# Kernel optimization log

Hardware: AMD Instinct MI355X
Metric: run time of the kernel (lower is better)

Reference implementation:

```python
import jax, jax.numpy as jnp
import numpy as np
from jax import lax

NUM_CLASSES = 80
STRIDES = (8, 16, 32)
CENTER_RADIUS = 2.5
CANDIDATE_K = 10


def setup_inputs() -> dict:
    key = jax.random.key(0)
    ks = jax.random.split(key, 6)
    B, G, NGT = 32, 50, 20
    out0 = jax.random.normal(ks[0], (B, 85, 80, 80), jnp.float32)
    out1 = jax.random.normal(ks[1], (B, 85, 40, 40), jnp.float32)
    out2 = jax.random.normal(ks[2], (B, 85, 20, 20), jnp.float32)
    cls = jax.random.randint(ks[3], (B, G, 1), 0, NUM_CLASSES).astype(jnp.float32)
    cxcy = jax.random.uniform(ks[4], (B, G, 2), minval=32.0, maxval=608.0)
    wh = jax.random.uniform(ks[5], (B, G, 2), minval=16.0, maxval=128.0)
    labels = jnp.concatenate([cls, cxcy, wh], -1)
    valid = (jnp.arange(G) < NGT)[None, :, None]
    labels = labels * valid  # padded rows are all-zero, as the torch code expects
    return {"out0": out0, "out1": out1, "out2": out2, "labels": labels}


def _decode(out, stride):
    # out: [B, 85, H, W] -> [B, H*W, 85] with xy=(pred+grid)*stride, wh=exp(pred)*stride
    B, C, H, W = out.shape
    o = out.transpose(0, 2, 3, 1).reshape(B, H * W, C)
    yv, xv = jnp.meshgrid(jnp.arange(H), jnp.arange(W), indexing="ij")
    grid = jnp.stack([xv, yv], -1).reshape(H * W, 2).astype(out.dtype)
    xy = (o[..., :2] + grid) * stride
    wh = jnp.exp(o[..., 2:4]) * stride
    dec = jnp.concatenate([xy, wh, o[..., 4:]], -1)
    centers = (grid + 0.5) * stride
    strides = jnp.full((H * W,), float(stride), out.dtype)
    return dec, centers, strides


def _pairwise_iou(a, b):
    # a: [G,4] cxcywh, b: [A,4] cxcywh -> [G,A]
    tl = jnp.maximum(a[:, None, :2] - a[:, None, 2:] * 0.5, b[None, :, :2] - b[None, :, 2:] * 0.5)
    br = jnp.minimum(a[:, None, :2] + a[:, None, 2:] * 0.5, b[None, :, :2] + b[None, :, 2:] * 0.5)
    en = jnp.all(tl < br, -1).astype(a.dtype)
    inter = jnp.prod(br - tl, -1) * en
    area_a = a[:, 2] * a[:, 3]
    area_b = b[:, 2] * b[:, 3]
    return inter / (area_a[:, None] + area_b[None, :] - inter + 1e-12)


def _iou_loss(pred, tgt):
    # elementwise IoU loss (YOLOX IOUloss, loss_type='iou'): 1 - iou^2
    tl = jnp.maximum(pred[..., :2] - pred[..., 2:] * 0.5, tgt[..., :2] - tgt[..., 2:] * 0.5)
    br = jnp.minimum(pred[..., :2] + pred[..., 2:] * 0.5, tgt[..., :2] + tgt[..., 2:] * 0.5)
    en = jnp.all(tl < br, -1).astype(pred.dtype)
    inter = jnp.prod(jnp.clip(br - tl, 0.0), -1) * en
    union = pred[..., 2] * pred[..., 3] + tgt[..., 2] * tgt[..., 3] - inter + 1e-16
    iou = inter / union
    return 1.0 - iou * iou


def _bce_logits(x, y):
    return jnp.maximum(x, 0.0) - x * y + jnp.log1p(jnp.exp(-jnp.abs(x)))


def _assign(boxes, cls_logits, obj_logit, labels_b, centers, strides):
    # Per-image SimOTA. boxes [A,4], cls_logits [A,C], obj_logit [A], labels_b [G,5]
    G = labels_b.shape[0]
    gt_valid = labels_b.sum(-1) > 0                       # [G]
    gt_box = labels_b[:, 1:5]                             # [G,4] cxcywh
    gt_cls = labels_b[:, 0].astype(jnp.int32)
    cx, cy = centers[:, 0], centers[:, 1]
    # in-box test (strict, as min(delta)>0 in torch)
    in_box = ((cx[None] > gt_box[:, 0:1] - 0.5 * gt_box[:, 2:3])
              & (cx[None] < gt_box[:, 0:1] + 0.5 * gt_box[:, 2:3])
              & (cy[None] > gt_box[:, 1:2] - 0.5 * gt_box[:, 3:4])
              & (cy[None] < gt_box[:, 1:2] + 0.5 * gt_box[:, 3:4]))  # [G,A]
    rs = CENTER_RADIUS * strides[None]
    in_ctr = ((jnp.abs(cx[None] - gt_box[:, 0:1]) < rs)
              & (jnp.abs(cy[None] - gt_box[:, 1:2]) < rs))           # [G,A]
    fg = jnp.any((in_box | in_ctr) & gt_valid[:, None], axis=0)       # [A]
    geom = in_box & in_ctr                                            # is_in_boxes_and_center
    cand = fg[None, :] & gt_valid[:, None]                            # valid (gt, anchor) pairs

    iou = _pairwise_iou(gt_box, boxes)                                # [G,A]
    iou_m = jnp.where(cand, iou, 0.0)
    iou_cost = -jnp.log(iou + 1e-8)

    # cls cost without materializing [G,A,C]: p = sqrt(sig(cls)*sig(obj));
    # BCE(p, onehot(g)).sum(C) = -log p[g] + log(1-p[g]) - sum_c log(1-p[c])
    p = jnp.sqrt(jax.nn.sigmoid(cls_logits) * jax.nn.sigmoid(obj_logit)[:, None])  # [A,C]
    p = jnp.clip(p, 1e-7, 1.0 - 1e-6)
    logp = jnp.log(p)
    log1mp = jnp.log1p(-p)
    s = log1mp.sum(-1)                                                # [A]
    lp_g = jnp.take(logp, gt_cls, axis=1).T                           # [G,A]
    l1_g = jnp.take(log1mp, gt_cls, axis=1).T                         # [G,A]
    cls_cost = -lp_g + l1_g - s[None, :]

    cost = (cls_cost + 3.0 * iou_cost
            + 100000.0 * (~geom).astype(cost_dtype := boxes.dtype)
            + 1e9 * (~cand).astype(boxes.dtype))

    # dynamic-k: k_g = clamp(int(sum(topk10 ious)), 1)
    topk_ious = lax.top_k(iou_m, CANDIDATE_K)[0]                      # [G,10]
    dyn_k = jnp.clip(topk_ious.sum(-1).astype(jnp.int32), 1, None)    # [G]
    sorted_cost = jnp.sort(cost, axis=1)
    thr = jnp.take_along_axis(sorted_cost, (dyn_k - 1)[:, None], axis=1)
    match = (cost <= thr) & cand                                      # [G,A]

    # resolve anchors matched to multiple gts: keep global argmin-cost gt
    count = match.sum(0)                                              # [A]
    best_gt = jnp.argmin(cost, axis=0)                                # [A]
    keep = jnp.arange(G)[:, None] == best_gt[None, :]
    match = jnp.where(count[None, :] > 1, match & keep, match)

    fg_final = match.any(0)                                           # [A]
    matched_gt = jnp.argmax(match, axis=0)                            # [A]
    pred_iou = (match.astype(iou.dtype) * iou).sum(0)                 # [A]
    return fg_final, matched_gt, pred_iou, gt_valid


def _forward(out0, out1, out2, labels):
    decs, ctrs, strs = [], [], []
    for o, s in zip((out0, out1, out2), STRIDES):
        d, c, st = _decode(o, s)
        decs.append(d); ctrs.append(c); strs.append(st)
    outputs = jnp.concatenate(decs, axis=1)          # [B, A, 85]
    centers = jnp.concatenate(ctrs, axis=0)          # [A, 2]
    strides = jnp.concatenate(strs, axis=0)          # [A]

    bbox = outputs[..., :4]
    obj = outputs[..., 4]
    cls = outputs[..., 5:]

    assign = jax.vmap(_assign, in_axes=(0, 0, 0, 0, None, None))
    fg, mgt, piou, gt_valid = assign(
        lax.stop_gradient(bbox), lax.stop_gradient(cls),
        lax.stop_gradient(obj), lax.stop_gradient(labels), centers, strides)
    piou = lax.stop_gradient(piou)

    gt_box = lax.stop_gradient(labels[:, :, 1:5])
    reg_t = jnp.take_along_axis(gt_box, mgt[..., None], axis=1)       # [B,A,4]
    gt_cls = labels[..., 0].astype(jnp.int32)
    mcls = jnp.take_along_axis(gt_cls, mgt, axis=1)                   # [B,A]
    cls_t = jax.nn.one_hot(mcls, NUM_CLASSES, dtype=outputs.dtype) * piou[..., None]

    fgf = fg.astype(outputs.dtype)
    num_fg = jnp.maximum(fgf.sum(), 1.0)
    loss_iou = (_iou_loss(bbox, reg_t) * fgf).sum() / num_fg
    loss_obj = _bce_logits(obj, fgf).sum() / num_fg
    loss_cls = (_bce_logits(cls, cls_t).sum(-1) * fgf).sum() / num_fg
    return 5.0 * loss_iou + loss_obj + loss_cls


def reference(out0, out1, out2, labels):
    return _forward(out0, out1, out2, labels)
```

## Files before the change

kernel.cpp:

```cpp
#include <hip/hip_runtime.h>
#include <math.h>

#define B_  32
#define A_  8400
#define G_  50
#define NC_ 80
#define PAD 4352
#define CHK_A 33
#define CHK_C 17
#define NBLK_C (8*4*CHK_C)
#define CLIPHI ((float)(1.0 - 1e-6))

#define ACC_NUMFG 0
#define ACC_IOU   32
#define ACC_OBJ0  64
#define ACC_OBJFG 96
#define ACC_CLS   128

struct AInfo { int lvl; int within; int w; int hw; float s; int x; int y; };

__device__ __forceinline__ AInfo anchor_info(int a) {
  AInfo r;
  if (a < 6400)      { r.lvl = 0; r.within = a;        r.w = 80; r.hw = 6400; r.s = 8.0f;  }
  else if (a < 8000) { r.lvl = 1; r.within = a - 6400; r.w = 40; r.hw = 1600; r.s = 16.0f; }
  else               { r.lvl = 2; r.within = a - 8000; r.w = 20; r.hw = 400;  r.s = 32.0f; }
  r.x = r.within % r.w; r.y = r.within / r.w;
  return r;
}

__device__ __forceinline__ const float* lvl_base(const float* o0, const float* o1,
                                                 const float* o2, int lvl) {
  return lvl == 0 ? o0 : (lvl == 1 ? o1 : o2);
}

__device__ __forceinline__ float2 cost_iou(
    float gx, float gy, float gw, float gh,
    float fx, float fy, float st,
    float4 bx, float ssum, float sobj, float clsv)
{
  float cx = (fx + 0.5f) * st;
  float cy = (fy + 0.5f) * st;
  bool in_box = (cx > gx - 0.5f*gw) && (cx < gx + 0.5f*gw) &&
                (cy > gy - 0.5f*gh) && (cy < gy + 0.5f*gh);
  float rs = 2.5f * st;
  bool in_ctr = (fabsf(cx - gx) < rs) && (fabsf(cy - gy) < rs);
  bool geom = in_box && in_ctr;
  float tlx = fmaxf(gx - gw*0.5f, bx.x - bx.z*0.5f);
  float tly = fmaxf(gy - gh*0.5f, bx.y - bx.w*0.5f);
  float brx = fminf(gx + gw*0.5f, bx.x + bx.z*0.5f);
  float bry = fminf(gy + gh*0.5f, bx.y + bx.w*0.5f);
  bool en = (tlx < brx) && (tly < bry);
  float inter = en ? (brx - tlx) * (bry - tly) : 0.0f;
  float iou = inter / (gw*gh + bx.z*bx.w - inter + 1e-12f);
  float iou_cost = -__logf(iou + 1e-8f);
  float sc = 1.0f / (1.0f + __expf(-clsv));
  float p = sqrtf(sc * sobj);
  p = fminf(fmaxf(p, 1e-7f), CLIPHI);
  float cls_cost = -__logf(p) + __logf(1.0f - p) - ssum;
  float cost = cls_cost + 3.0f * iou_cost;
  if (!geom) cost += 100000.0f;
  return make_float2(cost, iou);
}

__global__ __launch_bounds__(256)
void kA(const float* __restrict__ o0, const float* __restrict__ o1,
        const float* __restrict__ o2, const float* __restrict__ labels,
        float4* __restrict__ cBox, float4* __restrict__ cPack,
        int* __restrict__ ncandP, float* __restrict__ accP)
{
  __shared__ float gl[G_], gr[G_], gtt[G_], gbb[G_], gcx[G_], gcy[G_];
  __shared__ int nvgS;
  __shared__ float wsum[4];
  __shared__ int wcnt[4], wbase[4];
  __shared__ int aL[256];
  __shared__ float soL[256], v4L[256];
  int j = blockIdx.x;
  int x8 = j & 7, r = j >> 3;
  int b = x8 + 8*(r & 3);
  int chunk = r >> 2;
  int tid = threadIdx.x;
  if (tid < 64) {
    bool v = false; float l0=0,gx=0,gy=0,gw=0,gh=0;
    if (tid < G_) {
      const float* L = labels + (size_t)b*G_*5 + tid*5;
      l0=L[0]; gx=L[1]; gy=L[2]; gw=L[3]; gh=L[4];
      v = (l0+gx+gy+gw+gh) > 0.0f;
    }
    unsigned long long mm = __ballot(v);
    if (tid == 0) nvgS = __popcll(mm);
    if (v) {
      int pos = __popcll(mm & ((1ull << tid) - 1ull));
      gl[pos]  = gx - 0.5f*gw; gr[pos]  = gx + 0.5f*gw;
      gtt[pos] = gy - 0.5f*gh; gbb[pos] = gy + 0.5f*gh;
      gcx[pos] = gx; gcy[pos] = gy;
    }
  }
  __syncthreads();
  int nvg = nvgS;
  int a = chunk*256 + tid;
  float objbce = 0.0f, v4 = 0.0f, so = 0.0f;
  float4 bx = make_float4(0.f,0.f,0.f,0.f);
  bool anyfg = false;
  if (a < A_) {
    AInfo ai = anchor_info(a);
    const float* base = lvl_base(o0,o1,o2,ai.lvl) + (size_t)b*85*ai.hw + ai.within;
    float v0 = base[0];
    float v1 = base[(size_t)1*ai.hw];
    float v2 = base[(size_t)2*ai.hw];
    float v3 = base[(size_t)3*ai.hw];
    v4 = base[(size_t)4*ai.hw];
    bx.x = (v0 + (float)ai.x) * ai.s;
    bx.y = (v1 + (float)ai.y) * ai.s;
    bx.z = __expf(v2) * ai.s;
    bx.w = __expf(v3) * ai.s;
    objbce = fmaxf(v4, 0.0f) + __logf(1.0f + __expf(-fabsf(v4)));
    float cx = ((float)ai.x + 0.5f) * ai.s;
    float cy = ((float)ai.y + 0.5f) * ai.s;
    float rs = 2.5f * ai.s;
    for (int k = 0; k < nvg; k++) {
      bool in_box = (cx > gl[k]) & (cx < gr[k]) & (cy > gtt[k]) & (cy < gbb[k]);
      bool in_ctr = (fabsf(cx - gcx[k]) < rs) & (fabsf(cy - gcy[k]) < rs);
      anyfg = anyfg | in_box | in_ctr;
    }
    so = 1.0f / (1.0f + __expf(-v4));
  }
  float v = objbce;
  for (int o = 32; o > 0; o >>= 1) v += __shfl_down(v, o, 64);
  int lane = tid & 63, w = tid >> 6;
  if (lane == 0) wsum[w] = v;
  unsigned long long mm = __ballot(anyfg);
  if (lane == 0) wcnt[w] = __popcll(mm);
  __syncthreads();
  if (tid == 0) {
    atomicAdd(&accP[ACC_OBJ0], wsum[0]+wsum[1]+wsum[2]+wsum[3]);
    int t0=wcnt[0], t1=wcnt[1], t2=wcnt[2], t3=wcnt[3];
    int tot = t0+t1+t2+t3;
    int bas = tot ? atomicAdd(&ncandP[b*64], tot) : 0;
    wbase[0]=bas; wbase[1]=bas+t0; wbase[2]=bas+t0+t1; wbase[3]=bas+t0+t1+t2;
  }
  __syncthreads();
  if (anyfg) {
    int pre = __popcll(mm & ((1ull << lane) - 1ull));
    int lpos = (wbase[w] - wbase[0]) + pre;
    aL[lpos] = a; soL[lpos] = so; v4L[lpos] = v4;
    int pos = wbase[w] + pre;
    if (pos < PAD) cBox[b*PAD + pos] = bx;
  }
  __syncthreads();
  int base0 = wbase[0];
  int tot = (wbase[3] + wcnt[3]) - base0;
  for (int t = tid; t < tot; t += 256) {
    if (base0 + t >= PAD) break;
    int a2 = aL[t];
    float so2 = soL[t];
    AInfo ai = anchor_info(a2);
    const float* q = lvl_base(o0,o1,o2,ai.lvl) + (size_t)(b*85 + 5)*ai.hw + ai.within;
    float s0=0,s1=0,s2=0,s3=0,s4=0,s5=0,s6=0,s7=0;
    #pragma unroll
    for (int c = 0; c < NC_; c += 8) {
      float x0 = q[(size_t)(c+0)*ai.hw];
      float x1 = q[(size_t)(c+1)*ai.hw];
      float x2 = q[(size_t)(c+2)*ai.hw];
      float x3 = q[(size_t)(c+3)*ai.hw];
      float x4 = q[(size_t)(c+4)*ai.hw];
      float x5 = q[(size_t)(c+5)*ai.hw];
      float x6 = q[(size_t)(c+6)*ai.hw];
      float x7 = q[(size_t)(c+7)*ai.hw];
      #define TERM(xx, ss_) { \
        float sc = 1.0f/(1.0f+__expf(-(xx))); \
        float p = sqrtf(sc*so2); \
        p = fminf(fmaxf(p,1e-7f), CLIPHI); \
        ss_ += __logf(1.0f - p); }
      TERM(x0,s0) TERM(x1,s1) TERM(x2,s2) TERM(x3,s3)
      TERM(x4,s4) TERM(x5,s5) TERM(x6,s6) TERM(x7,s7)
      #undef TERM
    }
    float ss = ((s0+s1)+(s2+s3)) + ((s4+s5)+(s6+s7));
    cPack[b*PAD + base0 + t] = make_float4(ss, so2, __int_as_float(a2), v4L[t]);
  }
}

__global__ __launch_bounds__(256)
void kB(const float* __restrict__ o0, const float* __restrict__ o1,
        const float* __restrict__ o2, const float* __restrict__ labels,
        const float4* __restrict__ cBox, const float4* __restrict__ cPack,
        const int* __restrict__ ncandP, float* __restrict__ thrw,
        float* __restrict__ costM)
{
  __shared__ float sh[256*10];
  __shared__ int s_dk;
  int j = blockIdx.x;
  int x8 = j & 7, r = j >> 3;
  int b = x8 + 8*(r & 3);
  int g = r >> 2;
  int tid = threadIdx.x;
  const float* L = labels + (size_t)(b*G_ + g)*5;
  float l0=L[0], gx=L[1], gy=L[2], gw=L[3], gh=L[4];
  bool gvalid = (l0+gx+gy+gw+gh) > 0.0f;
  if (!gvalid) { if (tid==0) thrw[b*G_+g] = -3.0e38f; return; }
  int gcls = (int)l0;
  int nc = ncandP[b*64]; if (nc > PAD) nc = PAD;
  float* row = costM + ((size_t)b*G_ + g)*(size_t)PAD;
  float ti[10], tc[10];
  #pragma unroll
  for (int jq=0;jq<10;jq++){ ti[jq]=0.0f; tc[jq]=3e38f; }

  auto body = [&](int i) {
    float4 bx = cBox[b*PAD + i];
    float4 pk = cPack[b*PAD + i];
    int a = __float_as_int(pk.z);
    AInfo ai = anchor_info(a);
    float clsv = lvl_base(o0,o1,o2,ai.lvl)[(size_t)(b*85 + 5 + gcls)*ai.hw + ai.within];
    float2 ci = cost_iou(gx,gy,gw,gh,(float)ai.x,(float)ai.y,ai.s,
                         bx, pk.x, pk.y, clsv);
    row[i] = ci.x;
    float v = ci.y;
    if (v > ti[9]) {
      #pragma unroll
      for (int jq=0;jq<10;jq++){ float o=ti[jq]; bool t=v>o; ti[jq]=t?v:o; v=t?o:v; }
    }
    float c = ci.x;
    if (c < tc[9]) {
      #pragma unroll
      for (int jq=0;jq<10;jq++){ float o=tc[jq]; bool t=c<o; tc[jq]=t?c:o; c=t?o:c; }
    }
  };
  int i = tid;
  for (; i + 256 < nc; i += 512) { body(i); body(i + 256); }
  if (i < nc) body(i);

  #pragma unroll
  for (int jq=0;jq<10;jq++) sh[tid*10+jq] = ti[jq];
  __syncthreads();
  for (int str=128; str>0; str>>=1) {
    if (tid < str) {
      float out[10]; int ii=0, jj=0;
      float* Aa = &sh[tid*10]; float* Bb = &sh[(tid+str)*10];
      #pragma unroll
      for (int k=0;k<10;k++){ float va=Aa[ii], vb=Bb[jj]; bool t=(va>=vb); out[k]=t?va:vb; if(t)ii++; else jj++; }
      #pragma unroll
      for (int k=0;k<10;k++) Aa[k]=out[k];
    }
    __syncthreads();
  }
  if (tid==0) {
    float s10=0.0f;
    #pragma unroll
    for (int jq=0;jq<10;jq++) s10 += sh[jq];
    int dk = (int)s10; if (dk<1) dk=1; if (dk>10) dk=10;
    s_dk = dk;
  }
  __syncthreads();
  #pragma unroll
  for (int jq=0;jq<10;jq++) sh[tid*10+jq] = tc[jq];
  __syncthreads();
  for (int str=128; str>0; str>>=1) {
    if (tid < str) {
      float out[10]; int ii=0, jj=0;
      float* Aa = &sh[tid*10]; float* Bb = &sh[(tid+str)*10];
      #pragma unroll
      for (int k=0;k<10;k++){ float va=Aa[ii], vb=Bb[jj]; bool t=(va<=vb); out[k]=t?va:vb; if(t)ii++; else jj++; }
      #pragma unroll
      for (int k=0;k<10;k++) Aa[k]=out[k];
    }
    __syncthreads();
  }
  if (tid==0) thrw[b*G_+g] = sh[s_dk-1];
}

__global__ __launch_bounds__(256)
void kC(const float* __restrict__ o0, const float* __restrict__ o1,
        const float* __restrict__ o2, const float* __restrict__ labels,
        const float4* __restrict__ cBox, const float4* __restrict__ cPack,
        const int* __restrict__ ncandP, const float* __restrict__ thrw,
        const float* __restrict__ costM, float* __restrict__ accP,
        int* __restrict__ doneP, float* __restrict__ out)
{
  __shared__ float labS[G_*5];
  __shared__ float thrS[G_];
  __shared__ int vgIdx[G_];
  __shared__ int nvgS;
  __shared__ float wpart[4][4];
  __shared__ int aML[256];
  __shared__ float piML[256];
  __shared__ int mclsML[256];
  __shared__ int mcntS;
  int j = blockIdx.x;
  int x8 = j & 7, r = j >> 3;
  int b = x8 + 8*(r & 3);
  int chunk = r >> 2;
  int tid = threadIdx.x;
  int nc = ncandP[b*64]; if (nc > PAD) nc = PAD;
  bool active = (chunk*256 < nc);
  if (active) {
    for (int i = tid; i < G_*5; i += 256) labS[i] = labels[(size_t)b*G_*5 + i];
    if (tid < G_) thrS[tid] = thrw[b*G_ + tid];
    if (tid == 0) mcntS = 0;
    __syncthreads();
    if (tid < 64) {
      bool v = false;
      if (tid < G_) {
        float s5 = labS[tid*5]+labS[tid*5+1]+labS[tid*5+2]+labS[tid*5+3]+labS[tid*5+4];
        v = (s5 > 0.0f);
      }
      unsigned long long mm = __ballot(v);
      if (tid == 0) nvgS = __popcll(mm);
      if (v) vgIdx[__popcll(mm & ((1ull << tid) - 1ull))] = tid;
    }
    __syncthreads();
    int nvg = nvgS;
    int i = chunk*256 + tid;
    float accPf=0.f, accIou=0.f, accObjx=0.f, accCls=0.f;
    bool matched = false; int m_a = 0; float m_pi = 0.0f; int m_cls = 0;
    if (i < nc) {
      const float* cm = costM + (size_t)b*G_*(size_t)PAD + i;
      float minc = 3e38f; int ming = 0;
      int cnt = 0; int firstg = -1;
      #define PROC(kk, cc) { \
        int g = vgIdx[kk]; \
        if ((cc) < minc) { minc = (cc); ming = g; } \
        if ((cc) <= thrS[g]) { cnt++; if (firstg < 0) firstg = g; } }
      int k = 0;
      for (; k + 4 <= nvg; k += 4) {
        float c0 = cm[(size_t)vgIdx[k+0]*PAD];
        float c1 = cm[(size_t)vgIdx[k+1]*PAD];
        float c2 = cm[(size_t)vgIdx[k+2]*PAD];
        float c3 = cm[(size_t)vgIdx[k+3]*PAD];
        PROC(k+0, c0) PROC(k+1, c1) PROC(k+2, c2) PROC(k+3, c3)
      }
      for (; k < nvg; k++) {
        float c0 = cm[(size_t)vgIdx[k]*PAD];
        PROC(k, c0)
      }
      #undef PROC
      int mg = -1;
      if (cnt == 1)     mg = firstg;
      else if (cnt > 1) { if (minc <= thrS[ming]) mg = ming; }
      if (mg >= 0) {
        float4 bx = cBox[b*PAD + i];
        float4 pk = cPack[b*PAD + i];
        accPf = 1.0f;
        accObjx = pk.w;
        float tx=labS[mg*5+1], ty=labS[mg*5+2], tw=labS[mg*5+3], th=labS[mg*5+4];
        float tlx = fmaxf(tx - tw*0.5f, bx.x - bx.z*0.5f);
        float tly = fmaxf(ty - th*0.5f, bx.y - bx.w*0.5f);
        float brx = fminf(tx + tw*0.5f, bx.x + bx.z*0.5f);
        float bry = fminf(ty + th*0.5f, bx.y + bx.w*0.5f);
        bool en = (tlx < brx) && (tly < bry);
        float inter_p = en ? (brx - tlx) * (bry - tly) : 0.0f;
        float pi = inter_p / (tw*th + bx.z*bx.w - inter_p + 1e-12f);
        float iw = fmaxf(brx-tlx, 0.0f), ih = fmaxf(bry-tly, 0.0f);
        float inter = iw*ih * (en ? 1.0f : 0.0f);
        float uni = bx.z*bx.w + tw*th - inter + 1e-16f;
        float iou2 = inter/uni;
        accIou = 1.0f - iou2*iou2;
        matched = true;
        m_a = __float_as_int(pk.z);
        m_pi = pi;
        m_cls = (int)labS[mg*5];
      }
    }
    {
      int lane = tid & 63;
      unsigned long long mm = __ballot(matched);
      int cnt = __popcll(mm);
      int bpos = 0;
      if (lane == 0 && cnt) bpos = atomicAdd(&mcntS, cnt);
      bpos = __shfl(bpos, 0, 64);
      if (matched) {
        int p = bpos + __popcll(mm & ((1ull << lane) - 1ull));
        aML[p] = m_a; piML[p] = m_pi; mclsML[p] = m_cls;
      }
    }
    __syncthreads();
    {
      int lane = tid & 63, w = tid >> 6;
      int mcount = mcntS;
      for (int idx = w; idx < mcount; idx += 4) {
        int a2 = aML[idx]; float pi2 = piML[idx]; int mc = mclsML[idx];
        AInfo ai = anchor_info(a2);
        const float* clsbase = lvl_base(o0,o1,o2,ai.lvl) + (size_t)(b*85 + 5)*ai.hw + ai.within;
        float x1 = clsbase[(size_t)lane * ai.hw];
        accCls += fmaxf(x1,0.0f) - x1*((lane==mc)?pi2:0.0f) + __logf(1.0f + __expf(-fabsf(x1)));
        if (lane < NC_ - 64) {
          int c2 = lane + 64;
          float x2 = clsbase[(size_t)c2 * ai.hw];
          accCls += fmaxf(x2,0.0f) - x2*((c2==mc)?pi2:0.0f) + __logf(1.0f + __expf(-fabsf(x2)));
        }
      }
    }
    for (int o = 32; o > 0; o >>= 1) {
      accPf   += __shfl_down(accPf,   o, 64);
      accIou  += __shfl_down(accIou,  o, 64);
      accObjx += __shfl_down(accObjx, o, 64);
      accCls  += __shfl_down(accCls,  o, 64);
    }
    int lane = tid & 63, w = tid >> 6;
    if (lane == 0) { wpart[w][0]=accPf; wpart[w][1]=accIou; wpart[w][2]=accObjx; wpart[w][3]=accCls; }
    __syncthreads();
    if (tid == 0) {
      float s0=0.f,s1=0.f,s2=0.f,s3=0.f;
      for (int q=0;q<4;q++){ s0+=wpart[q][0]; s1+=wpart[q][1]; s2+=wpart[q][2]; s3+=wpart[q][3]; }
      if (s0!=0.f) atomicAdd(&accP[ACC_NUMFG], s0);
      if (s1!=0.f) atomicAdd(&accP[ACC_IOU],   s1);
      if (s2!=0.f) atomicAdd(&accP[ACC_OBJFG], s2);
      if (s3!=0.f) atomicAdd(&accP[ACC_CLS],   s3);
    }
  }
  if (tid == 0) {
    __threadfence();
    int old = atomicAdd(doneP, 1);
    if (old == NBLK_C - 1) {
      float nfg  = atomicAdd(&accP[ACC_NUMFG], 0.0f);
      float liou = atomicAdd(&accP[ACC_IOU],   0.0f);
      float obj0 = atomicAdd(&accP[ACC_OBJ0],  0.0f);
      float objf = atomicAdd(&accP[ACC_OBJFG], 0.0f);
      float lcls = atomicAdd(&accP[ACC_CLS],   0.0f);
      float nf = fmaxf(nfg, 1.0f);
      out[0] = (5.0f*liou + (obj0 - objf) + lcls) / nf;
    }
  }
}

extern "C" void kernel_launch(void* const* d_in, const int* in_sizes, int n_in,
                              void* d_out, int out_size, void* d_ws, size_t ws_size,
                              hipStream_t stream)
{
  const float* o0 = (const float*)d_in[0];
  const float* o1 = (const float*)d_in[1];
  const float* o2 = (const float*)d_in[2];
  const float* labels = (const float*)d_in[3];
  char* w = (char*)d_ws;
  size_t off = 0;
  auto alloc = [&](size_t bytes) -> void* {
    void* p = w + off; off += (bytes + 255) & ~(size_t)255; return p;
  };
  char*  ctrl  = (char*)alloc(8192 + 1024 + 256);
  int*   ncandP= (int*)ctrl;
  float* accP  = (float*)(ctrl + 8192);
  int*   doneP = (int*)(ctrl + 8192 + 1024);
  float4* cBox  = (float4*)alloc(sizeof(float4)*(size_t)B_*PAD);
  float4* cPack = (float4*)alloc(sizeof(float4)*(size_t)B_*PAD);
  float*  thrw  = (float*) alloc(sizeof(float)*(size_t)B_*G_);
  float*  costM = (float*) alloc(sizeof(float)*(size_t)B_*G_*(size_t)PAD);

  hipMemsetAsync(ctrl, 0, 8192 + 1024 + 256, stream);

  kA<<<8*4*CHK_A, 256, 0, stream>>>(o0,o1,o2,labels,cBox,cPack,ncandP,accP);
  kB<<<8*4*G_,    256, 0, stream>>>(o0,o1,o2,labels,cBox,cPack,ncandP,thrw,costM);
  kC<<<NBLK_C,    256, 0, stream>>>(o0,o1,o2,labels,cBox,cPack,ncandP,thrw,costM,accP,doneP,(float*)d_out);
}
```

Measured before the change: 181.4 us.

## Split candidate class-sum computation into separate compacted kernel for load balance

Moves the per-candidate sum over 80 class log terms out of the anchor-scan kernel into a new kernel that indexes the compacted candidate list per batch. The scan kernel now writes candidate metadata straight to the packed buffer and exits. This aims to remove thread imbalance, where chunks with few candidates left most lanes idle. In exchange it adds a kernel launch and an extra round trip of the packed buffer through global memory.

```diff
diff --git a/kernel.cpp b/kernel.cpp
--- a/kernel.cpp
+++ b/kernel.cpp
@@ -63,17 +63,15 @@
 }
 
 __global__ __launch_bounds__(256)
-void kA(const float* __restrict__ o0, const float* __restrict__ o1,
-        const float* __restrict__ o2, const float* __restrict__ labels,
-        float4* __restrict__ cBox, float4* __restrict__ cPack,
-        int* __restrict__ ncandP, float* __restrict__ accP)
+void kA1(const float* __restrict__ o0, const float* __restrict__ o1,
+         const float* __restrict__ o2, const float* __restrict__ labels,
+         float4* __restrict__ cBox, float4* __restrict__ cPack,
+         int* __restrict__ ncandP, float* __restrict__ accP)
 {
   __shared__ float gl[G_], gr[G_], gtt[G_], gbb[G_], gcx[G_], gcy[G_];
   __shared__ int nvgS;
   __shared__ float wsum[4];
   __shared__ int wcnt[4], wbase[4];
-  __shared__ int aL[256];
-  __shared__ float soL[256], v4L[256];
   int j = blockIdx.x;
   int x8 = j & 7, r = j >> 3;
   int b = x8 + 8*(r & 3);
@@ -141,43 +139,54 @@
   __syncthreads();
   if (anyfg) {
     int pre = __popcll(mm & ((1ull << lane) - 1ull));
-    int lpos = (wbase[w] - wbase[0]) + pre;
-    aL[lpos] = a; soL[lpos] = so; v4L[lpos] = v4;
     int pos = wbase[w] + pre;
-    if (pos < PAD) cBox[b*PAD + pos] = bx;
-  }
-  __syncthreads();
-  int base0 = wbase[0];
-  int tot = (wbase[3] + wcnt[3]) - base0;
-  for (int t = tid; t < tot; t += 256) {
-    if (base0 + t >= PAD) break;
-    int a2 = aL[t];
-    float so2 = soL[t];
-    AInfo ai = anchor_info(a2);
-    const float* q = lvl_base(o0,o1,o2,ai.lvl) + (size_t)(b*85 + 5)*ai.hw + ai.within;
-    float s0=0,s1=0,s2=0,s3=0,s4=0,s5=0,s6=0,s7=0;
-    #pragma unroll
-    for (int c = 0; c < NC_; c += 8) {
-      float x0 = q[(size_t)(c+0)*ai.hw];
-      float x1 = q[(size_t)(c+1)*ai.hw];
-      float x2 = q[(size_t)(c+2)*ai.hw];
-      float x3 = q[(size_t)(c+3)*ai.hw];
-      float x4 = q[(size_t)(c+4)*ai.hw];
-      float x5 = q[(size_t)(c+5)*ai.hw];
-      float x6 = q[(size_t)(c+6)*ai.hw];
-      float x7 = q[(size_t)(c+7)*ai.hw];
-      #define TERM(xx, ss_) { \
-        float sc = 1.0f/(1.0f+__expf(-(xx))); \
-        float p = sqrtf(sc*so2); \
-        p = fminf(fmaxf(p,1e-7f), CLIPHI); \
-        ss_ += __logf(1.0f - p); }
-      TERM(x0,s0) TERM(x1,s1) TERM(x2,s2) TERM(x3,s3)
-      TERM(x4,s4) TERM(x5,s5) TERM(x6,s6) TERM(x7,s7)
-      #undef TERM
-    }
-    float ss = ((s0+s1)+(s2+s3)) + ((s4+s5)+(s6+s7));
-    cPack[b*PAD + base0 + t] = make_float4(ss, so2, __int_as_float(a2), v4L[t]);
-  }
+    if (pos < PAD) {
+      cBox[b*PAD + pos]  = bx;
+      cPack[b*PAD + pos] = make_float4(0.0f, so, __int_as_float(a), v4);
+    }
+  }
+}
+
+__global__ __launch_bounds__(256)
+void kA2(const float* __restrict__ o0, const float* __restrict__ o1,
+         const float* __restrict__ o2, float4* __restrict__ cPack,
+         const int* __restrict__ ncandP)
+{
+  int j = blockIdx.x;
+  int x8 = j & 7, r = j >> 3;
+  int b = x8 + 8*(r & 3);
+  int chunk = r >> 2;
+  int tid = threadIdx.x;
+  int nc = ncandP[b*64]; if (nc > PAD) nc = PAD;
+  int i = chunk*256 + tid;
+  if (i >= nc) return;
+  float4 pk = cPack[b*PAD + i];
+  int a2 = __float_as_int(pk.z);
+  float so2 = pk.y;
+  AInfo ai = anchor_info(a2);
+  const float* q = lvl_base(o0,o1,o2,ai.lvl) + (size_t)(b*85 + 5)*ai.hw + ai.within;
+  float s0=0,s1=0,s2=0,s3=0,s4=0,s5=0,s6=0,s7=0;
+  #pragma unroll
+  for (int c = 0; c < NC_; c += 8) {
+    float x0 = q[(size_t)(c+0)*ai.hw];
+    float x1 = q[(size_t)(c+1)*ai.hw];
+    float x2 = q[(size_t)(c+2)*ai.hw];
+    float x3 = q[(size_t)(c+3)*ai.hw];
+    float x4 = q[(size_t)(c+4)*ai.hw];
+    float x5 = q[(size_t)(c+5)*ai.hw];
+    float x6 = q[(size_t)(c+6)*ai.hw];
+    float x7 = q[(size_t)(c+7)*ai.hw];
+    #define TERM(xx, ss_) { \
+      float sc = 1.0f/(1.0f+__expf(-(xx))); \
+      float p = sqrtf(sc*so2); \
+      p = fminf(fmaxf(p,1e-7f), CLIPHI); \
+      ss_ += __logf(1.0f - p); }
+    TERM(x0,s0) TERM(x1,s1) TERM(x2,s2) TERM(x3,s3)
+    TERM(x4,s4) TERM(x5,s5) TERM(x6,s6) TERM(x7,s7)
+    #undef TERM
+  }
+  float ss = ((s0+s1)+(s2+s3)) + ((s4+s5)+(s6+s7));
+  cPack[b*PAD + i].x = ss;
 }
 
 __global__ __launch_bounds__(256)
@@ -446,7 +455,8 @@
 
   hipMemsetAsync(ctrl, 0, 8192 + 1024 + 256, stream);
 
-  kA<<<8*4*CHK_A, 256, 0, stream>>>(o0,o1,o2,labels,cBox,cPack,ncandP,accP);
-  kB<<<8*4*G_,    256, 0, stream>>>(o0,o1,o2,labels,cBox,cPack,ncandP,thrw,costM);
-  kC<<<NBLK_C,    256, 0, stream>>>(o0,o1,o2,labels,cBox,cPack,ncandP,thrw,costM,accP,doneP,(float*)d_out);
-}
+  kA1<<<8*4*CHK_A, 256, 0, stream>>>(o0,o1,o2,labels,cBox,cPack,ncandP,accP);
+  kA2<<<8*4*CHK_C, 256, 0, stream>>>(o0,o1,o2,cPack,ncandP);
+  kB <<<8*4*G_,    256, 0, stream>>>(o0,o1,o2,labels,cBox,cPack,ncandP,thrw,costM);
+  kC <<<NBLK_C,    256, 0, stream>>>(o0,o1,o2,labels,cBox,cPack,ncandP,thrw,costM,accP,doneP,(float*)d_out);
+}
```

Result: slower. 191.4 us (+5.5%).
